# Optimization experiments

Hardware: AMD Instinct MI355X
Metric: run time of the kernel (lower is better)

## Reference

```python
import jax, jax.numpy as jnp
import numpy as np

B = 32; N = 16; Hn = 4; Wn = 4; P = 64; EPS = 1e-5
INV_SQRT2 = 0.7071067811865476

def _conv3x3(x, w, stride):
    # x: [B,Cin,H,W], w: [Cout,Cin,3,3]; torch Conv2d(k=3, padding=1, bias=False)
    return jax.lax.conv_general_dilated(x, w, (stride, stride), ((1, 1), (1, 1)),
                                        dimension_numbers=('NCHW', 'OIHW', 'NCHW'))

def _herpn(x, w):
    # HerPN activation: per-channel batch-norm (batch stats, biased var) followed by
    # a degree-2 normalized probabilist-Hermite expansion with learned coeffs w: [3,C].
    mu = x.mean((0, 2, 3), keepdims=True)
    var = x.var((0, 2, 3), keepdims=True)
    xh = (x - mu) * jax.lax.rsqrt(var + EPS)
    w0 = w[0][:, None, None]; w1 = w[1][:, None, None]; w2 = w[2][:, None, None]
    return w0 + w1 * xh + w2 * (xh * xh - 1.0) * INV_SQRT2

def _backbone(xp, c0, h1, c1, h2, c2, h3, c3, h4, c4, h5, c5, ph, g, b):
    # xp: [B,3,64,64] -> [B,256]
    out = _conv3x3(xp, c0, 1)
    for h, c, s in ((h1, c1, 1), (h2, c2, 2), (h3, c3, 1), (h4, c4, 2), (h5, c5, 1)):
        out = _conv3x3(_herpn(out, h), c, s)
    out = _herpn(out, ph)                              # [B,64,16,16]
    Bp, C, Hs, Ws = out.shape
    out = out.reshape(Bp, C, 2, Hs // 2, 2, Ws // 2).mean((3, 5))  # adaptive avg pool -> (2,2)
    out = out.reshape(Bp, -1)                          # [B,256]
    mu = out.mean(0); var = out.var(0)                 # BatchNorm1d (batch stats)
    return (out - mu) * jax.lax.rsqrt(var + EPS) * g + b

def setup_inputs():
    key = jax.random.key(0)
    ks = jax.random.split(key, 20)
    rn = lambda i, shp, s=0.1: jax.random.normal(ks[i], shp, jnp.float32) * s
    return {
        'x': jax.random.normal(ks[0], (B, 3, 256, 256), jnp.float32),
        'conv0_w': rn(1, (N, 16, 3, 3, 3), 0.25),
        'hw1': rn(2, (N, 3, 16), 0.5), 'cw1': rn(3, (N, 16, 16, 3, 3), 0.12),
        'hw2': rn(4, (N, 3, 16), 0.5), 'cw2': rn(5, (N, 32, 16, 3, 3), 0.12),
        'hw3': rn(6, (N, 3, 32), 0.5), 'cw3': rn(7, (N, 32, 32, 3, 3), 0.08),
        'hw4': rn(8, (N, 3, 32), 0.5), 'cw4': rn(9, (N, 64, 32, 3, 3), 0.08),
        'hw5': rn(10, (N, 3, 64), 0.5), 'cw5': rn(11, (N, 64, 64, 3, 3), 0.06),
        'pool_hw': rn(12, (N, 3, 64), 0.5),
        'bn1_g': jnp.ones((N, 256), jnp.float32),
        'bn1_b': jnp.zeros((N, 256), jnp.float32),
        'lin_w': rn(13, (256, N * 256), 0.02),
        'lin_b': jnp.zeros((256,), jnp.float32),
        'jig_w': rn(14, (N, 256), 0.05),
        'jig_b': jnp.zeros((N,), jnp.float32),
    }

def reference(x, conv0_w, hw1, cw1, hw2, cw2, hw3, cw3, hw4, cw4, hw5, cw5,
              pool_hw, bn1_g, bn1_b, lin_w, lin_b, jig_w, jig_b):
    # rearrange: b c (h p1) (w p2) -> (h w) b c p1 p2
    patches = x.reshape(B, 3, Hn, P, Wn, P).transpose(2, 4, 0, 1, 3, 5).reshape(N, B, 3, P, P)
    # fused grouped computation: vmap over the N distinct-weight backbones
    y = jax.vmap(_backbone)(patches, conv0_w, hw1, cw1, hw2, cw2, hw3, cw3,
                            hw4, cw4, hw5, cw5, pool_hw, bn1_g, bn1_b)  # [N,B,256]
    out = y.transpose(1, 0, 2)                       # [B,N,256]
    og = out.reshape(B, -1) @ lin_w.T + lin_b        # [B,256]
    og = (og - og.mean(0)) * jax.lax.rsqrt(og.var(0) + EPS)  # BN affine=False
    pred = (jnp.einsum('bnc,kc->bnk', out, jig_w) + jig_b).reshape(-1, N)  # [B*N,N]
    target = jnp.tile(jnp.arange(N), B)
    return og, pred, target
```

## Files before the change

kernel.cpp:

```cpp
#include <hip/hip_runtime.h>
#include <hip/hip_bf16.h>

typedef __hip_bfloat16 bf16;

#define BB 32
#define NN 16
#define NSH 16

using bf16x8v = __attribute__((ext_vector_type(8))) short;
using f32x4v  = __attribute__((ext_vector_type(4))) float;

__device__ __forceinline__ float b2f(bf16 v){ return __bfloat162float(v); }
__device__ __forceinline__ bf16  f2b(float v){ return __float2bfloat16(v); }
__device__ __forceinline__ float bfbits2f(unsigned int h){
    unsigned int x = h << 16; float f; __builtin_memcpy(&f, &x, 4); return f;
}
__device__ __forceinline__ unsigned bbits(float f){
    bf16 h = f2b(f); unsigned short u; __builtin_memcpy(&u, &h, 2); return (unsigned)u;
}
__device__ __forceinline__ bf16x8v pack8(float4 a, float4 b){
    bf16x8v r;
    r[0] = (short)bbits(a.x); r[1] = (short)bbits(a.y);
    r[2] = (short)bbits(a.z); r[3] = (short)bbits(a.w);
    r[4] = (short)bbits(b.x); r[5] = (short)bbits(b.y);
    r[6] = (short)bbits(b.z); r[7] = (short)bbits(b.w);
    return r;
}

__launch_bounds__(256)
__global__ void detect_ker(const uint4* __restrict__ xs, int* __restrict__ flag)
{
    const int base = blockIdx.x * 1024 + threadIdx.x;
    int cnt = 0;
    #pragma unroll
    for (int k = 0; k < 4; ++k) {
        uint4 v = xs[base + k * 256];
        unsigned w[4] = {v.x, v.y, v.z, v.w};
        #pragma unroll
        for (int p = 0; p < 4; ++p) {
            if ((w[p] & 0x7F80u) == 0x7F80u) cnt++;
            if (((w[p] >> 16) & 0x7F80u) == 0x7F80u) cnt++;
        }
    }
    unsigned long long m = __ballot(cnt != 0);
    if ((threadIdx.x & 63) == 0 && m != 0ull) atomicOr(flag, 1);
}

struct CvtArgs { const void* src[19]; int cnt[19]; int off[19]; };

__launch_bounds__(256)
__global__ void convert_ker(CvtArgs a, float* __restrict__ dst, const int* __restrict__ flag)
{
    const int which = blockIdx.y;
    const int cnt = a.cnt[which];
    if ((int)blockIdx.x * 2048 >= cnt) return;
    const int base = blockIdx.x * 2048 + threadIdx.x;
    float* d = dst + a.off[which];
    if (*flag) {
        const float* s = (const float*)a.src[which];
        #pragma unroll
        for (int k = 0; k < 8; ++k) { int j = base + k * 256; if (j < cnt) d[j] = s[j]; }
    } else {
        const bf16* s = (const bf16*)a.src[which];
        #pragma unroll
        for (int k = 0; k < 8; ++k) { int j = base + k * 256; if (j < cnt) d[j] = b2f(s[j]); }
    }
}

struct WpArgs { const float* src[5]; bf16* dst[5]; int cout[5]; int cin[5]; int nk[5]; int tot[5]; };

__launch_bounds__(256)
__global__ void wprep_ker(WpArgs a)
{
    const int stg = blockIdx.y;
    const int cout = a.cout[stg], cin = a.cin[stg], nk = a.nk[stg];
    int idx = blockIdx.x * 256 + threadIdx.x;
    if (idx >= a.tot[stg]) return;
    int j  = idx & 7;
    int co = (idx >> 3) % cout;
    int rest = (idx >> 3) / cout;
    int k8 = rest & 3;
    int cn = rest >> 2;
    int c  = cn % nk;
    int n  = cn / nk;
    int k  = c * 32 + k8 * 8 + j;
    int tap = k / cin;
    int ci  = k - tap * cin;
    float v = 0.f;
    if (tap < 9) v = a.src[stg][((size_t)(n * cout + co) * cin + ci) * 9 + tap];
    a.dst[stg][idx] = f2b(v);
}

__launch_bounds__(256)
__global__ void conv0w_ker(const float* __restrict__ x, const float* __restrict__ w,
                           bf16* __restrict__ a0, float* __restrict__ accum)
{
    constexpr int STRIP = 8, STRIPS = 8, IN_ROWS = 10, TW = 66;
    constexpr int G = NN * BB * STRIPS;
    __shared__ float tile[3][IN_ROWS][TW];
    const int tid = threadIdx.x;
    const int bid = (blockIdx.x & 7) * (G >> 3) + (blockIdx.x >> 3);
    const int st = bid % STRIPS;
    const int b = (bid / STRIPS) % BB;
    const int n = bid / (STRIPS * BB);
    const int pr = (n >> 2) * 64, pc = (n & 3) * 64;
    const int r0 = st * STRIP - 1;

    for (int idx = tid; idx < 3 * IN_ROWS * TW; idx += 256) {
        int ci = idx / (IN_ROWS * TW);
        int rem = idx - ci * (IN_ROWS * TW);
        int rr = rem / TW, cc = rem - rr * TW;
        int gr = r0 + rr, gc = cc - 1;
        float v = 0.f;
        if (gr >= 0 && gr < 64 && gc >= 0 && gc < 64)
            v = x[((size_t)(b * 3 + ci) * 256 + (pr + gr)) * 256 + (pc + gc)];
        tile[ci][rr][cc] = v;
    }
    __syncthreads();

    const int xo = tid & 63;
    const int wv = tid >> 6;
    const int co0 = wv * 4;
    const float* wb = w + __builtin_amdgcn_readfirstlane((n * 16 + co0) * 27);

    float acc[4][STRIP];
    #pragma unroll
    for (int t = 0; t < 4; ++t)
        #pragma unroll
        for (int r = 0; r < STRIP; ++r) acc[t][r] = 0.f;

    #pragma unroll
    for (int ci = 0; ci < 3; ++ci) {
        float wr[4][9];
        #pragma unroll
        for (int t = 0; t < 4; ++t)
            #pragma unroll
            for (int j = 0; j < 9; ++j)
                wr[t][j] = wb[t * 27 + ci * 9 + j];
        float win[3][3];
        #pragma unroll
        for (int c0 = 0; c0 < 3; ++c0) {
            win[0][c0] = tile[ci][0][xo + c0];
            win[1][c0] = tile[ci][1][xo + c0];
        }
        #pragma unroll
        for (int ry = 0; ry < STRIP; ++ry) {
            #pragma unroll
            for (int c0 = 0; c0 < 3; ++c0)
                win[(ry + 2) % 3][c0] = tile[ci][ry + 2][xo + c0];
            #pragma unroll
            for (int ky = 0; ky < 3; ++ky)
                #pragma unroll
                for (int kx = 0; kx < 3; ++kx) {
                    float v = win[(ry + ky) % 3][kx];
                    #pragma unroll
                    for (int t = 0; t < 4; ++t)
                        acc[t][ry] = fmaf(v, wr[t][ky * 3 + kx], acc[t][ry]);
                }
        }
    }

    bf16* ab = a0 + (size_t)(n * BB + b) * 65536 + (size_t)st * 8192;
    #pragma unroll
    for (int r = 0; r < STRIP; ++r) {
        uint2 pk;
        pk.x = (bbits(acc[1][r]) << 16) | bbits(acc[0][r]);
        pk.y = (bbits(acc[3][r]) << 16) | bbits(acc[2][r]);
        *(uint2*)&ab[(size_t)(r * 64 + xo) * 16 + co0] = pk;
    }

    float s[4], q[4];
    #pragma unroll
    for (int t = 0; t < 4; ++t) {
        s[t] = 0.f; q[t] = 0.f;
        #pragma unroll
        for (int r = 0; r < STRIP; ++r) {
            s[t] += acc[t][r];
            q[t] = fmaf(acc[t][r], acc[t][r], q[t]);
        }
    }
    #pragma unroll
    for (int off = 32; off > 0; off >>= 1) {
        #pragma unroll
        for (int t = 0; t < 4; ++t) {
            s[t] += __shfl_down(s[t], off, 64);
            q[t] += __shfl_down(q[t], off, 64);
        }
    }
    if (xo == 0) {
        float* As = accum + (bid & (NSH - 1)) * (2 * NN * 16);
        #pragma unroll
        for (int t = 0; t < 4; ++t) {
            atomicAdd(&As[n * 16 + co0 + t],           s[t]);
            atomicAdd(&As[256 + n * 16 + co0 + t], q[t]);
        }
    }
}

template<int CIN, int COUT, int WIN, int STRIDE, int RB>
__launch_bounds__(256)
__global__ void mconv_ker(const bf16* __restrict__ ain, const float* __restrict__ aprev,
                          const float* __restrict__ hw, const bf16* __restrict__ wt,
                          bf16* __restrict__ aout, float* __restrict__ accum)
{
    constexpr int HIN = WIN;
    constexpr int WOUT = WIN / STRIDE, HOUT = WIN / STRIDE;
    constexpr int CIN8 = CIN / 8;
    constexpr int XS = WIN + 2;
    constexpr int IN_ROWS = STRIDE * (RB - 1) + 3;
    constexpr int STRIPS = HOUT / RB;
    constexpr int G = NN * BB * STRIPS;
    constexpr int NK = (CIN == 16) ? 5 : (9 * CIN) / 32;
    constexpr int NT = COUT / 16;
    constexpr int MT = RB * (WOUT / 16);
    constexpr int MW = MT / 4;
    constexpr int SW = (CIN8 == 2) ? 2 : ((CIN8 == 4) ? 1 : 0);
    constexpr int SM = CIN8 - 1;
    static_assert(MT % 4 == 0, "4 waves");
    static_assert(G % 8 == 0, "bijective XCD swizzle");

    __shared__ __align__(16) short tile[IN_ROWS * XS * CIN8 * 8];
    __shared__ float cfA[CIN], cfB[CIN], cfC[CIN];
    __shared__ float sred[2][COUT];

    const int tid = threadIdx.x;
    const int bid = (blockIdx.x & 7) * (G >> 3) + (blockIdx.x >> 3);
    const int st = bid % STRIPS;
    const int b = (bid / STRIPS) % BB;
    const int n = bid / (STRIPS * BB);

    if (tid < CIN) {
        constexpr float cinv = 1.f / (float)(BB * WIN * WIN);
        float ssum = 0.f, sq = 0.f;
        #pragma unroll
        for (int sh = 0; sh < NSH; ++sh) {
            ssum += aprev[sh * 2 * NN * CIN + n * CIN + tid];
            sq   += aprev[sh * 2 * NN * CIN + NN * CIN + n * CIN + tid];
        }
        float mu = ssum * cinv;
        float var = fmaxf(sq * cinv - mu * mu, 0.f);
        float rs = rsqrtf(var + 1e-5f);
        float w0 = hw[(n * 3 + 0) * CIN + tid];
        float w1 = hw[(n * 3 + 1) * CIN + tid];
        float w2 = hw[(n * 3 + 2) * CIN + tid];
        float c2 = w2 * 0.70710678118654752440f;
        float rs2 = rs * rs;
        cfA[tid] = (w0 - c2) - w1 * rs * mu + c2 * rs2 * mu * mu;
        cfB[tid] = w1 * rs - 2.f * c2 * rs2 * mu;
        cfC[tid] = c2 * rs2;
    }
    if (tid < 2 * COUT) ((float*)sred)[tid] = 0.f;
    __syncthreads();

    const int r0 = st * RB * STRIDE - 1;
    const bf16* abase = ain + (size_t)(n * BB + b) * (HIN * WIN * CIN);

    {
        uint4 z4; z4.x = 0u; z4.y = 0u; z4.z = 0u; z4.w = 0u;
        for (int h = tid; h < IN_ROWS * 2 * CIN8; h += 256) {
            int c8 = h % CIN8;
            int t = h / CIN8;
            int xs = (t & 1) ? (XS - 1) : 0;
            int rr = t >> 1;
            int i16 = (rr * XS + xs) * CIN8 + (c8 ^ ((xs >> SW) & SM));
            *(uint4*)&tile[i16 * 8] = z4;
        }
    }
    for (int h = tid; h < IN_ROWS * WIN * CIN8; h += 256) {
        int c8 = h % CIN8;
        int t = h / CIN8;
        int xx = t % WIN;
        int rr = t / WIN;
        int gr = r0 + rr;
        uint4 pk; pk.x = 0u; pk.y = 0u; pk.z = 0u; pk.w = 0u;
        if (gr >= 0 && gr < HIN) {
            uint4 raw = *(const uint4*)(abase + ((size_t)gr * WIN + xx) * CIN + c8 * 8);
            unsigned rw[4] = {raw.x, raw.y, raw.z, raw.w};
            unsigned ou[4];
            #pragma unroll
            for (int p = 0; p < 4; ++p) {
                int ci0 = c8 * 8 + p * 2;
                float v0 = bfbits2f(rw[p] & 0xffffu);
                float v1 = bfbits2f(rw[p] >> 16);
                v0 = fmaf(v0, fmaf(v0, cfC[ci0],     cfB[ci0]),     cfA[ci0]);
                v1 = fmaf(v1, fmaf(v1, cfC[ci0 + 1], cfB[ci0 + 1]), cfA[ci0 + 1]);
                ou[p] = (bbits(v1) << 16) | bbits(v0);
            }
            pk.x = ou[0]; pk.y = ou[1]; pk.z = ou[2]; pk.w = ou[3];
        }
        int xs = xx + 1;
        int i16 = (rr * XS + xs) * CIN8 + (c8 ^ ((xs >> SW) & SM));
        *(uint4*)&tile[i16 * 8] = pk;
    }
    __syncthreads();

    const int lane = tid & 63;
    const int wv = tid >> 6;
    const int qq = lane >> 4;
    const int ln = lane & 15;

    int idxc[NK];
    #pragma unroll
    for (int c = 0; c < NK; ++c) {
        int tap, c8;
        if (CIN == 16)      { tap = 2 * c + (qq >> 1); c8 = qq & 1; if (tap > 8) tap = 0; }
        else if (CIN == 32) { tap = c;                 c8 = qq; }
        else                { tap = c >> 1;            c8 = ((c & 1) << 2) | qq; }
        int dy = tap / 3, dx = tap - dy * 3;
        int xs = ln * STRIDE + dx;
        idxc[c] = (dy * XS + xs) * CIN8 + (c8 ^ ((xs >> SW) & SM));
    }

    const bf16* wbase = wt + (size_t)n * (NK * 4 * COUT * 8);
    const bf16x8v zv = {0, 0, 0, 0, 0, 0, 0, 0};

    for (int nt = 0; nt < NT; ++nt) {
        const int co0 = nt * 16;
        bf16x8v Bf[NK];
        #pragma unroll
        for (int c = 0; c < NK; ++c)
            Bf[c] = *(const bf16x8v*)(wbase + ((size_t)(c * 4 + qq) * COUT + co0 + ln) * 8);
        float sA = 0.f, sQ = 0.f;
        for (int i = 0; i < MW; ++i) {
            const int mt = wv * MW + i;
            const int orow = mt / (WOUT / 16);
            const int x0 = (mt % (WOUT / 16)) * 16;
            const int moff = (orow * STRIDE * XS + x0 * STRIDE) * CIN8;
            f32x4v acc = {0.f, 0.f, 0.f, 0.f};
            #pragma unroll
            for (int c = 0; c < NK; ++c) {
                bf16x8v av = *(const bf16x8v*)&tile[(idxc[c] + moff) * 8];
                if (CIN == 16 && c == NK - 1) {
                    if (qq & 2) av = zv;
                }
                acc = __builtin_amdgcn_mfma_f32_16x16x32_bf16(av, Bf[c], acc, 0, 0, 0);
            }
            float s1 = acc[0] + acc[1] + acc[2] + acc[3];
            float q1 = fmaf(acc[0], acc[0], fmaf(acc[1], acc[1],
                       fmaf(acc[2], acc[2], acc[3] * acc[3])));
            s1 += __shfl_xor(s1, 16, 64); s1 += __shfl_xor(s1, 32, 64);
            q1 += __shfl_xor(q1, 16, 64); q1 += __shfl_xor(q1, 32, 64);
            sA += s1; sQ += q1;
            bf16* ob = aout + (((size_t)(n * BB + b) * HOUT + (st * RB + orow)) * WOUT + x0) * COUT
                       + co0 + ln;
            #pragma unroll
            for (int r = 0; r < 4; ++r)
                ob[(qq * 4 + r) * COUT] = f2b(acc[r]);
        }
        if (qq == 0) {
            atomicAdd(&sred[0][co0 + ln], sA);
            atomicAdd(&sred[1][co0 + ln], sQ);
        }
    }
    __syncthreads();
    {
        float* As = accum + (bid & (NSH - 1)) * (2 * NN * COUT);
        for (int t2 = tid; t2 < COUT; t2 += 256) {
            atomicAdd(&As[n * COUT + t2], sred[0][t2]);
            atomicAdd(&As[NN * COUT + n * COUT + t2], sred[1][t2]);
        }
    }
}

__launch_bounds__(256)
__global__ void pool_ker(const bf16* __restrict__ a5, const float* __restrict__ aprev,
                         const float* __restrict__ hw, float* __restrict__ y)
{
    const int n = blockIdx.x / BB, b = blockIdx.x % BB;
    const int f = threadIdx.x;
    const int c = f & 63, qd = f >> 6, qh = qd >> 1, qw = qd & 1;
    const bf16* p = a5 + (size_t)(n * BB + b) * 16384;
    const float cinv = 1.f / 8192.f;
    float ssum0 = 0.f, sq0 = 0.f;
    #pragma unroll
    for (int sh = 0; sh < NSH; ++sh) {
        ssum0 += aprev[sh * 2 * NN * 64 + n * 64 + c];
        sq0   += aprev[sh * 2 * NN * 64 + NN * 64 + n * 64 + c];
    }
    float mu = ssum0 * cinv;
    float var = fmaxf(sq0 * cinv - mu * mu, 0.f);
    float rs = rsqrtf(var + 1e-5f);
    float w0 = hw[(n * 3 + 0) * 64 + c];
    float w1 = hw[(n * 3 + 1) * 64 + c];
    float w2 = hw[(n * 3 + 2) * 64 + c];
    float c2 = w2 * 0.70710678118654752440f;
    float rs2 = rs * rs;
    float A  = (w0 - c2) - w1 * rs * mu + c2 * rs2 * mu * mu;
    float Bc = w1 * rs - 2.f * c2 * rs2 * mu;
    float Cc = c2 * rs2;
    float ssum = 0.f;
    for (int iy = 0; iy < 8; ++iy)
        for (int ix = 0; ix < 8; ++ix) {
            float raw = b2f(p[(size_t)((qh * 8 + iy) * 16 + (qw * 8 + ix)) * 64 + c]);
            ssum += fmaf(raw, fmaf(raw, Cc, Bc), A);
        }
    y[(size_t)(n * BB + b) * 256 + c * 4 + qh * 2 + qw] = ssum * (1.f / 64.f);
}

__launch_bounds__(256)
__global__ void bn1_ker(const float* __restrict__ y, const float* __restrict__ g,
                        const float* __restrict__ bta, float* __restrict__ yt)
{
    const int gid = blockIdx.x * 256 + threadIdx.x;
    const int n = gid >> 8;
    float s = 0.f, s2 = 0.f;
    for (int b = 0; b < BB; ++b) {
        float v = y[(size_t)((n * BB + b) * 256) + (gid & 255)];
        s += v;
        s2 = fmaf(v, v, s2);
    }
    float mu = s * (1.f / BB);
    float var = fmaxf(s2 * (1.f / BB) - mu * mu, 0.f);
    float rs = rsqrtf(var + 1e-5f);
    float gg = g[gid];
    float bb = bta[gid];
    for (int b = 0; b < BB; ++b) {
        float v = y[(size_t)((n * BB + b) * 256) + (gid & 255)];
        yt[(size_t)b * 4096 + gid] = fmaf((v - mu) * rs, gg, bb);
    }
}

__launch_bounds__(256)
__global__ void og_mm_ker(const float* __restrict__ yt, const float* __restrict__ lin_w,
                          void* __restrict__ d_out, const int* __restrict__ flag)
{
    __shared__ float part[4][32][17];
    const int tid = threadIdx.x;
    const int wv = tid >> 6;
    const int lane = tid & 63;
    const int qq = lane >> 4;
    const int ln = lane & 15;
    const int j0 = blockIdx.x * 16;

    const float* wrow  = lin_w + (size_t)(j0 + ln) * 4096 + wv * 1024;
    const float* yrow0 = yt + (size_t)ln * 4096 + wv * 1024;
    const float* yrow1 = yt + (size_t)(16 + ln) * 4096 + wv * 1024;

    f32x4v acc0 = {0.f, 0.f, 0.f, 0.f}, acc1 = {0.f, 0.f, 0.f, 0.f};
    for (int kc = 0; kc < 32; ++kc) {
        const int ko = kc * 32 + qq * 8;
        bf16x8v Bf = pack8(*(const float4*)(wrow + ko), *(const float4*)(wrow + ko + 4));
        bf16x8v A0 = pack8(*(const float4*)(yrow0 + ko), *(const float4*)(yrow0 + ko + 4));
        bf16x8v A1 = pack8(*(const float4*)(yrow1 + ko), *(const float4*)(yrow1 + ko + 4));
        acc0 = __builtin_amdgcn_mfma_f32_16x16x32_bf16(A0, Bf, acc0, 0, 0, 0);
        acc1 = __builtin_amdgcn_mfma_f32_16x16x32_bf16(A1, Bf, acc1, 0, 0, 0);
    }
    #pragma unroll
    for (int r = 0; r < 4; ++r) {
        part[wv][qq * 4 + r][ln]      = acc0[r];
        part[wv][16 + qq * 4 + r][ln] = acc1[r];
    }
    __syncthreads();

    if (tid < 16) {
        float vsum = 0.f, vsq = 0.f;
        for (int b = 0; b < BB; ++b) {
            float v = part[0][b][tid] + part[1][b][tid] + part[2][b][tid] + part[3][b][tid];
            vsum += v; vsq = fmaf(v, v, vsq);
        }
        float mu = vsum * (1.f / BB);
        float var = fmaxf(vsq * (1.f / BB) - mu * mu, 0.f);
        float rs = rsqrtf(var + 1e-5f);
        const int j = j0 + tid;
        const bool isf32 = (*flag != 0);
        for (int b = 0; b < BB; ++b) {
            float v = part[0][b][tid] + part[1][b][tid] + part[2][b][tid] + part[3][b][tid];
            float o = (v - mu) * rs;
            if (isf32) ((float*)d_out)[b * 256 + j] = o;
            else       ((bf16*)d_out)[b * 256 + j] = f2b(o);
        }
        float t = (float)(j & 15);
        if (isf32) { ((float*)d_out)[16384 + j] = t; ((float*)d_out)[16640 + j] = t; }
        else       { ((bf16*)d_out)[16384 + j] = f2b(t); ((bf16*)d_out)[16640 + j] = f2b(t); }
    }
}

__launch_bounds__(256)
__global__ void pred_ker(const float* __restrict__ yt, const float* __restrict__ jig_w,
                         const float* __restrict__ jig_b, void* __restrict__ d_out,
                         const int* __restrict__ flag)
{
    __shared__ float sy[256];
    const int b = blockIdx.x >> 4, n = blockIdx.x & 15;
    sy[threadIdx.x] = yt[(size_t)b * 4096 + n * 256 + threadIdx.x];
    __syncthreads();
    const int k = threadIdx.x >> 4, part = threadIdx.x & 15;
    const float* wrow = jig_w + k * 256 + part * 16;
    const float* srow = sy + part * 16;
    float p = 0.f;
    #pragma unroll
    for (int t = 0; t < 16; ++t) p = fmaf(srow[t], wrow[t], p);
    #pragma unroll
    for (int off = 8; off > 0; off >>= 1) p += __shfl_down(p, off, 16);
    if (part == 0) {
        float v = p + jig_b[k];
        int pidx = 8192 + (b * 16 + n) * 16 + k;
        if (*flag) ((float*)d_out)[pidx] = v;
        else       ((bf16*)d_out)[pidx] = f2b(v);
    }
}

extern "C" void kernel_launch(void* const* d_in, const int* in_sizes, int n_in,
                              void* d_out, int out_size, void* d_ws, size_t ws_size,
                              hipStream_t stream)
{
    char* wsb = (char*)d_ws;
    int*   flag   = (int*)wsb;
    float* y      = (float*)(wsb + 131072);
    float* yt     = (float*)(wsb + 655360);
    bf16*  wtb    = (bf16*)(wsb + 1310720);
    float* accumZ = (float*)(wsb + 3670016);
    float* staged = (float*)(wsb + 6029312);

    float* A0 = accumZ + 0;
    float* A1 = accumZ + 8192;
    float* A2 = accumZ + 16384;
    float* A3 = accumZ + 32768;
    float* A4 = accumZ + 49152;
    float* A5 = accumZ + 81920;

    bf16* wt1b = wtb;
    bf16* wt2b = wt1b + 40960;
    bf16* wt3b = wt2b + 81920;
    bf16* wt4b = wt3b + 147456;
    bf16* wt5b = wt4b + 294912;

    CvtArgs ca;
    int off = 0, maxc = 0;
    for (int i = 0; i < 19; ++i) {
        ca.src[i] = d_in[i];
        ca.cnt[i] = in_sizes[i];
        ca.off[i] = off;
        off += in_sizes[i];
        if (in_sizes[i] > maxc) maxc = in_sizes[i];
    }
    float* sx      = staged + ca.off[0];
    float* scw0    = staged + ca.off[1];
    float* shw1    = staged + ca.off[2];
    float* scw1    = staged + ca.off[3];
    float* shw2    = staged + ca.off[4];
    float* scw2    = staged + ca.off[5];
    float* shw3    = staged + ca.off[6];
    float* scw3    = staged + ca.off[7];
    float* shw4    = staged + ca.off[8];
    float* scw4    = staged + ca.off[9];
    float* shw5    = staged + ca.off[10];
    float* scw5    = staged + ca.off[11];
    float* spool   = staged + ca.off[12];
    float* sg      = staged + ca.off[13];
    float* sb      = staged + ca.off[14];
    float* slin_w  = staged + ca.off[15];
    float* slin_b  = staged + ca.off[16];
    float* sjig_w  = staged + ca.off[17];
    float* sjig_b  = staged + ca.off[18];
    (void)slin_b;

    size_t stagedEnd = 6029312ull + (size_t)off * 4ull;
    size_t r1off = (stagedEnd + (1ull << 20)) & ~((1ull << 20) - 1ull);

    hipMemsetAsync(flag, 0, 4, stream);
    detect_ker<<<32, 256, 0, stream>>>((const uint4*)d_in[0], flag);
    convert_ker<<<dim3((maxc + 2047) / 2048, 19), 256, 0, stream>>>(ca, staged, flag);

    WpArgs wp;
    wp.src[0] = scw1; wp.dst[0] = wt1b; wp.cout[0] = 16; wp.cin[0] = 16; wp.nk[0] = 5;  wp.tot[0] = 16*5*4*16*8;
    wp.src[1] = scw2; wp.dst[1] = wt2b; wp.cout[1] = 32; wp.cin[1] = 16; wp.nk[1] = 5;  wp.tot[1] = 16*5*4*32*8;
    wp.src[2] = scw3; wp.dst[2] = wt3b; wp.cout[2] = 32; wp.cin[2] = 32; wp.nk[2] = 9;  wp.tot[2] = 16*9*4*32*8;
    wp.src[3] = scw4; wp.dst[3] = wt4b; wp.cout[3] = 64; wp.cin[3] = 32; wp.nk[3] = 9;  wp.tot[3] = 16*9*4*64*8;
    wp.src[4] = scw5; wp.dst[4] = wt5b; wp.cout[4] = 64; wp.cin[4] = 64; wp.nk[4] = 18; wp.tot[4] = 16*18*4*64*8;
    wprep_ker<<<dim3(2304, 5), 256, 0, stream>>>(wp);

    hipMemsetAsync(accumZ, 0, 114688 * sizeof(float), stream);

    char* rA = wsb + r1off;
    char* rB = wsb + r1off + (64ull << 20);
    bf16* a0 = (bf16*)rB;
    bf16* a1 = (bf16*)rA;
    bf16* a2 = (bf16*)rB;
    bf16* a3 = (bf16*)rA;
    bf16* a4 = (bf16*)rB;
    bf16* a5 = (bf16*)rA;

    conv0w_ker<<<NN * BB * 8, 256, 0, stream>>>(sx, scw0, a0, A0);
    mconv_ker<16, 16, 64, 1, 8><<<NN * BB * 8, 256, 0, stream>>>(a0, A0, shw1, wt1b, a1, A1);
    mconv_ker<16, 32, 64, 2, 8><<<NN * BB * 4, 256, 0, stream>>>(a1, A1, shw2, wt2b, a2, A2);
    mconv_ker<32, 32, 32, 1, 8><<<NN * BB * 4, 256, 0, stream>>>(a2, A2, shw3, wt3b, a3, A3);
    mconv_ker<32, 64, 32, 2, 8><<<NN * BB * 2, 256, 0, stream>>>(a3, A3, shw4, wt4b, a4, A4);
    mconv_ker<64, 64, 16, 1, 16><<<NN * BB, 256, 0, stream>>>(a4, A4, shw5, wt5b, a5, A5);
    pool_ker<<<NN * BB, 256, 0, stream>>>(a5, A5, spool, y);

    bn1_ker<<<NN, 256, 0, stream>>>(y, sg, sb, yt);
    og_mm_ker<<<16, 256, 0, stream>>>(yt, slin_w, d_out, flag);
    pred_ker<<<BB * NN, 256, 0, stream>>>(yt, sjig_w, sjig_b, d_out, flag);
}
```

Before: 358.8 us.

## Split last conv's output-channel tiles across grid and chunk K to cut registers

```diff
diff --git a/kernel.cpp b/kernel.cpp
--- a/kernel.cpp
+++ b/kernel.cpp
@@ -197,8 +197,8 @@
     }
 }
 
-template<int CIN, int COUT, int WIN, int STRIDE, int RB>
-__launch_bounds__(256)
+template<int CIN, int COUT, int WIN, int STRIDE, int RB, int KCH, int MINW, bool SPLITNT>
+__launch_bounds__(256, MINW)
 __global__ void mconv_ker(const bf16* __restrict__ ain, const float* __restrict__ aprev,
                           const float* __restrict__ hw, const bf16* __restrict__ wt,
                           bf16* __restrict__ aout, float* __restrict__ accum)
@@ -218,6 +218,7 @@
     constexpr int SM = CIN8 - 1;
     static_assert(MT % 4 == 0, "4 waves");
     static_assert(G % 8 == 0, "bijective XCD swizzle");
+    static_assert(KCH == 0 || NK % KCH == 0, "K chunking divides NK");
 
     __shared__ __align__(16) short tile[IN_ROWS * XS * CIN8 * 8];
     __shared__ float cfA[CIN], cfB[CIN], cfC[CIN];
@@ -314,46 +315,110 @@
     const bf16* wbase = wt + (size_t)n * (NK * 4 * COUT * 8);
     const bf16x8v zv = {0, 0, 0, 0, 0, 0, 0, 0};
 
-    for (int nt = 0; nt < NT; ++nt) {
+    const int ntBeg = SPLITNT ? (int)blockIdx.y : 0;
+    const int ntEnd = SPLITNT ? ntBeg + 1 : NT;
+    for (int nt = ntBeg; nt < ntEnd; ++nt) {
         const int co0 = nt * 16;
-        bf16x8v Bf[NK];
-        #pragma unroll
-        for (int c = 0; c < NK; ++c)
-            Bf[c] = *(const bf16x8v*)(wbase + ((size_t)(c * 4 + qq) * COUT + co0 + ln) * 8);
-        float sA = 0.f, sQ = 0.f;
-        for (int i = 0; i < MW; ++i) {
-            const int mt = wv * MW + i;
-            const int orow = mt / (WOUT / 16);
-            const int x0 = (mt % (WOUT / 16)) * 16;
-            const int moff = (orow * STRIDE * XS + x0 * STRIDE) * CIN8;
-            f32x4v acc = {0.f, 0.f, 0.f, 0.f};
-            #pragma unroll
-            for (int c = 0; c < NK; ++c) {
-                bf16x8v av = *(const bf16x8v*)&tile[(idxc[c] + moff) * 8];
-                if (CIN == 16 && c == NK - 1) {
-                    if (qq & 2) av = zv;
+        if constexpr (KCH == 0) {
+            bf16x8v Bf[NK];
+            #pragma unroll
+            for (int c = 0; c < NK; ++c)
+                Bf[c] = *(const bf16x8v*)(wbase + ((size_t)(c * 4 + qq) * COUT + co0 + ln) * 8);
+            float sA = 0.f, sQ = 0.f;
+            for (int i = 0; i < MW; ++i) {
+                const int mt = wv * MW + i;
+                const int orow = mt / (WOUT / 16);
+                const int x0 = (mt % (WOUT / 16)) * 16;
+                const int moff = (orow * STRIDE * XS + x0 * STRIDE) * CIN8;
+                f32x4v acc = {0.f, 0.f, 0.f, 0.f};
+                #pragma unroll
+                for (int c = 0; c < NK; ++c) {
+                    bf16x8v av = *(const bf16x8v*)&tile[(idxc[c] + moff) * 8];
+                    if (CIN == 16 && c == NK - 1) {
+                        if (qq & 2) av = zv;
+                    }
+                    acc = __builtin_amdgcn_mfma_f32_16x16x32_bf16(av, Bf[c], acc, 0, 0, 0);
                 }
-                acc = __builtin_amdgcn_mfma_f32_16x16x32_bf16(av, Bf[c], acc, 0, 0, 0);
+                float s1 = acc[0] + acc[1] + acc[2] + acc[3];
+                float q1 = fmaf(acc[0], acc[0], fmaf(acc[1], acc[1],
+                           fmaf(acc[2], acc[2], acc[3] * acc[3])));
+                s1 += __shfl_xor(s1, 16, 64); s1 += __shfl_xor(s1, 32, 64);
+                q1 += __shfl_xor(q1, 16, 64); q1 += __shfl_xor(q1, 32, 64);
+                sA += s1; sQ += q1;
+                bf16* ob = aout + (((size_t)(n * BB + b) * HOUT + (st * RB + orow)) * WOUT + x0) * COUT
+                           + co0 + ln;
+                #pragma unroll
+                for (int r = 0; r < 4; ++r)
+                    ob[(qq * 4 + r) * COUT] = f2b(acc[r]);
             }
-            float s1 = acc[0] + acc[1] + acc[2] + acc[3];
-            float q1 = fmaf(acc[0], acc[0], fmaf(acc[1], acc[1],
-                       fmaf(acc[2], acc[2], acc[3] * acc[3])));
-            s1 += __shfl_xor(s1, 16, 64); s1 += __shfl_xor(s1, 32, 64);
-            q1 += __shfl_xor(q1, 16, 64); q1 += __shfl_xor(q1, 32, 64);
-            sA += s1; sQ += q1;
-            bf16* ob = aout + (((size_t)(n * BB + b) * HOUT + (st * RB + orow)) * WOUT + x0) * COUT
-                       + co0 + ln;
-            #pragma unroll
-            for (int r = 0; r < 4; ++r)
-                ob[(qq * 4 + r) * COUT] = f2b(acc[r]);
-        }
-        if (qq == 0) {
-            atomicAdd(&sred[0][co0 + ln], sA);
-            atomicAdd(&sred[1][co0 + ln], sQ);
+            if (qq == 0) {
+                atomicAdd(&sred[0][co0 + ln], sA);
+                atomicAdd(&sred[1][co0 + ln], sQ);
+            }
+        } else {
+            f32x4v accv[MW];
+            int moff[MW];
+            #pragma unroll
+            for (int i = 0; i < MW; ++i) {
+                const int mt = wv * MW + i;
+                const int orow = mt / (WOUT / 16);
+                const int x0 = (mt % (WOUT / 16)) * 16;
+                moff[i] = (orow * STRIDE * XS + x0 * STRIDE) * CIN8;
+                accv[i][0] = 0.f; accv[i][1] = 0.f; accv[i][2] = 0.f; accv[i][3] = 0.f;
+            }
+            #pragma unroll
+            for (int kc = 0; kc < NK / KCH; ++kc) {
+                bf16x8v Bf[KCH];
+                #pragma unroll
+                for (int c = 0; c < KCH; ++c)
+                    Bf[c] = *(const bf16x8v*)(wbase +
+                        ((size_t)((kc * KCH + c) * 4 + qq) * COUT + co0 + ln) * 8);
+                #pragma unroll
+                for (int i = 0; i < MW; ++i) {
+                    #pragma unroll
+                    for (int c = 0; c < KCH; ++c) {
+                        bf16x8v av = *(const bf16x8v*)&tile[(idxc[kc * KCH + c] + moff[i]) * 8];
+                        if (CIN == 16 && kc * KCH + c == NK - 1) {
+                            if (qq & 2) av = zv;
+                        }
+                        accv[i] = __builtin_amdgcn_mfma_f32_16x16x32_bf16(av, Bf[c], accv[i], 0, 0, 0);
+                    }
+                }
+            }
+            float sA = 0.f, sQ = 0.f;
+            #pragma unroll
+            for (int i = 0; i < MW; ++i) {
+                const int mt = wv * MW + i;
+                const int orow = mt / (WOUT / 16);
+                const int x0 = (mt % (WOUT / 16)) * 16;
+                f32x4v acc = accv[i];
+                float s1 = acc[0] + acc[1] + acc[2] + acc[3];
+                float q1 = fmaf(acc[0], acc[0], fmaf(acc[1], acc[1],
+                           fmaf(acc[2], acc[2], acc[3] * acc[3])));
+                s1 += __shfl_xor(s1, 16, 64); s1 += __shfl_xor(s1, 32, 64);
+                q1 += __shfl_xor(q1, 16, 64); q1 += __shfl_xor(q1, 32, 64);
+                sA += s1; sQ += q1;
+                bf16* ob = aout + (((size_t)(n * BB + b) * HOUT + (st * RB + orow)) * WOUT + x0) * COUT
+                           + co0 + ln;
+                #pragma unroll
+                for (int r = 0; r < 4; ++r)
+                    ob[(qq * 4 + r) * COUT] = f2b(acc[r]);
+            }
+            if (qq == 0) {
+                atomicAdd(&sred[0][co0 + ln], sA);
+                atomicAdd(&sred[1][co0 + ln], sQ);
+            }
         }
     }
     __syncthreads();
-    {
+    if constexpr (SPLITNT) {
+        float* As = accum + (bid & (NSH - 1)) * (2 * NN * COUT);
+        const int co0 = (int)blockIdx.y * 16;
+        if (tid < 16) {
+            atomicAdd(&As[n * COUT + co0 + tid], sred[0][co0 + tid]);
+            atomicAdd(&As[NN * COUT + n * COUT + co0 + tid], sred[1][co0 + tid]);
+        }
+    } else {
         float* As = accum + (bid & (NSH - 1)) * (2 * NN * COUT);
         for (int t2 = tid; t2 < COUT; t2 += 256) {
             atomicAdd(&As[n * COUT + t2], sred[0][t2]);
@@ -582,11 +647,11 @@
     bf16* a5 = (bf16*)rA;
 
     conv0w_ker<<<NN * BB * 8, 256, 0, stream>>>(sx, scw0, a0, A0);
-    mconv_ker<16, 16, 64, 1, 8><<<NN * BB * 8, 256, 0, stream>>>(a0, A0, shw1, wt1b, a1, A1);
-    mconv_ker<16, 32, 64, 2, 8><<<NN * BB * 4, 256, 0, stream>>>(a1, A1, shw2, wt2b, a2, A2);
-    mconv_ker<32, 32, 32, 1, 8><<<NN * BB * 4, 256, 0, stream>>>(a2, A2, shw3, wt3b, a3, A3);
-    mconv_ker<32, 64, 32, 2, 8><<<NN * BB * 2, 256, 0, stream>>>(a3, A3, shw4, wt4b, a4, A4);
-    mconv_ker<64, 64, 16, 1, 16><<<NN * BB, 256, 0, stream>>>(a4, A4, shw5, wt5b, a5, A5);
+    mconv_ker<16, 16, 64, 1, 8, 0, 1, false><<<NN * BB * 8, 256, 0, stream>>>(a0, A0, shw1, wt1b, a1, A1);
+    mconv_ker<16, 32, 64, 2, 8, 0, 1, false><<<NN * BB * 4, 256, 0, stream>>>(a1, A1, shw2, wt2b, a2, A2);
+    mconv_ker<32, 32, 32, 1, 8, 0, 1, false><<<NN * BB * 4, 256, 0, stream>>>(a2, A2, shw3, wt3b, a3, A3);
+    mconv_ker<32, 64, 32, 2, 8, 0, 1, false><<<NN * BB * 2, 256, 0, stream>>>(a3, A3, shw4, wt4b, a4, A4);
+    mconv_ker<64, 64, 16, 1, 16, 6, 3, true><<<dim3(NN * BB, 4), 256, 0, stream>>>(a4, A4, shw5, wt5b, a5, A5);
     pool_ker<<<NN * BB, 256, 0, stream>>>(a5, A5, spool, y);
 
     bn1_ker<<<NN, 256, 0, stream>>>(y, sg, sb, yt);
```

New measurement: 338.1 us. 5.8% less time.
